# Performance work log

Measured on AMD Instinct MI355X. Metric: run time of the kernel, lower is better.

The kernel has to match this reference:

```python
import jax, jax.numpy as jnp
import numpy as np

BATCH = 16384
NUM_INPUTS = 128
# features = squares (n) + singles (n) + pairs C(n,2)
NUM_FEATS = NUM_INPUTS + NUM_INPUTS + (NUM_INPUTS * (NUM_INPUTS - 1)) // 2  # 8384

# precompute pair index lists (equivalent to itertools.combinations(range(n), 2))
_II, _JJ = np.triu_indices(NUM_INPUTS, k=1)
_II = jnp.asarray(_II)
_JJ = jnp.asarray(_JJ)


def setup_inputs() -> dict:
    key = jax.random.key(0)
    k1, k2 = jax.random.split(key)
    x = jax.random.normal(k1, (BATCH, NUM_INPUTS), dtype=jnp.float32)
    w = jax.random.normal(k2, (NUM_FEATS,), dtype=jnp.float32) * 0.05
    return {"x": x, "w": w}


def reference(x, w):
    # order=2, with_squares=True
    # squares block: o=1 -> inputs**2 / 1**2
    sq = x * x
    # combination order 1: f = 1! -> x / 1
    singles = x
    # combination order 2: f = 2! -> x_i * x_j / 2 for all i<j (combinations order)
    pairs = (x[:, _II] * x[:, _JJ]) * jnp.float32(0.5)
    t = jnp.concatenate([sq, singles, pairs], axis=-1)  # [B, 8384]
    return t * w
```

## Files before the change

### kernel.cpp

```cpp
#include <hip/hip_runtime.h>


constexpr int BATCH   = 16384;
constexpr int NIN     = 128;
constexpr int NFEAT   = NIN + NIN + (NIN * (NIN - 1)) / 2;
constexpr int TPB     = 256;
constexpr int ROWS    = 8;
constexpr int RSTRIDE = 132;
constexpr int KITERS  = (NFEAT + TPB - 1) / TPB;

__device__ __forceinline__ int pair_off(int i) {
    return i * (NIN - 1) - (i * (i - 1)) / 2;
}

__device__ __forceinline__ void decode_f(int f, float w, int& i, int& j, float& ws) {
    if (f < NIN)          { i = f;       j = f;   ws = w; }
    else if (f < 2 * NIN) { i = f - NIN; j = NIN; ws = w; }
    else {
        const int p = f - 2 * NIN;
        float s = sqrtf((float)(65025 - 8 * p));
        int  ii = (int)((255.0f - s) * 0.5f);
        ii = min(max(ii, 0), NIN - 2);
        while (pair_off(ii + 1) <= p) ++ii;
        while (pair_off(ii)     >  p) --ii;
        i = ii; j = ii + 1 + (p - pair_off(ii));
        ws = w * 0.5f;
    }
}

__global__ void setup_kernel(const float* __restrict__ w,
                             float* __restrict__ wsb,
                             unsigned short* __restrict__ tbl) {
    const int f = blockIdx.x * TPB + threadIdx.x;
    if (f >= NFEAT) return;
    int i, j; float ws;
    decode_f(f, w[f], i, j, ws);
    wsb[f] = ws;
    tbl[f] = (unsigned short)((i << 8) | j);
}

template <bool USE_TBL>
__global__ __launch_bounds__(TPB) void cpl_kernel(const float* __restrict__ x,
                                                  const float* __restrict__ w,
                                                  const float* __restrict__ wsb,
                                                  const unsigned short* __restrict__ tbl,
                                                  float* __restrict__ out) {
    __shared__ float xs[ROWS * RSTRIDE];
    const int tid = threadIdx.x;
    const int r0  = blockIdx.x * ROWS;

    {
        const int r = tid >> 5, c = (tid & 31) * 4;
        float4 v = *reinterpret_cast<const float4*>(x + (size_t)(r0 + r) * NIN + c);
        *reinterpret_cast<float4*>(&xs[r * RSTRIDE + c]) = v;
    }
    if (tid < ROWS) xs[tid * RSTRIDE + NIN] = 1.0f;
    __syncthreads();

    unsigned short e_nx = 0; float w_nx = 0.0f;
    if (USE_TBL) { e_nx = tbl[tid]; w_nx = wsb[tid]; }

    for (int k = 0; k < KITERS; ++k) {
        const int f = k * TPB + tid;
        int i, j; float ws;
        if (USE_TBL) {
            const unsigned short e = e_nx; ws = w_nx;
            const int fn = min(f + TPB, NFEAT - 1);
            e_nx = tbl[fn]; w_nx = wsb[fn];
            i = e >> 8; j = e & 255;
        } else {
            if (f < NFEAT) decode_f(f, w[f], i, j, ws);
            else           { i = 0; j = 0; ws = 0.0f; }
        }
        if (f < NFEAT) {
            float* op = out + (size_t)r0 * NFEAT + f;
#pragma unroll
            for (int r = 0; r < ROWS; ++r) {
                const float* xr = &xs[r * RSTRIDE];
                op[(size_t)r * NFEAT] = xr[i] * xr[j] * ws;
            }
        }
    }
}

extern "C" void kernel_launch(void* const* d_in, const int* in_sizes, int n_in,
                              void* d_out, int out_size, void* d_ws, size_t ws_size,
                              hipStream_t stream) {
    const float* x = (const float*)d_in[0];
    const float* w = (const float*)d_in[1];
    float*     out = (float*)d_out;

    const size_t need = (size_t)NFEAT * sizeof(float) + (size_t)NFEAT * sizeof(unsigned short);
    float*          wsb = (float*)d_ws;
    unsigned short* tbl = (unsigned short*)((char*)d_ws + (size_t)NFEAT * sizeof(float));

    const dim3 grid(BATCH / ROWS);

    if (ws_size >= need) {
        setup_kernel<<<(NFEAT + TPB - 1) / TPB, TPB, 0, stream>>>(w, wsb, tbl);
        cpl_kernel<true><<<grid, TPB, 0, stream>>>(x, w, wsb, tbl, out);
    } else {
        cpl_kernel<false><<<grid, TPB, 0, stream>>>(x, w, wsb, tbl, out);
    }
}
```

Measured before the change: 115.5 us.

## Stage index/weight tables in shared memory and process 16 rows per block

Each block now copies the whole feature index table and scaled weights (about 67KB) into LDS, then iterates row-major over 16 batch rows instead of 8. Table lookups therefore come from LDS rather than from global/L2 on every feature iteration, and writes go out row by row. The cost is a large LDS footprint that limits occupancy to a block or two per CU, plus a per-block table copy, which may hurt latency hiding on a store-bound kernel.

```diff
diff --git a/kernel.cpp b/kernel.cpp
--- a/kernel.cpp
+++ b/kernel.cpp
@@ -1,21 +1,19 @@
 #include <hip/hip_runtime.h>
 
 
-constexpr int BATCH   = 16384;
-constexpr int NIN     = 128;
-constexpr int NFEAT   = NIN + NIN + (NIN * (NIN - 1)) / 2;
-constexpr int TPB     = 256;
-constexpr int ROWS    = 8;
-constexpr int RSTRIDE = 132;
-constexpr int KITERS  = (NFEAT + TPB - 1) / TPB;
+constexpr int BATCH = 16384;
+constexpr int NIN   = 128;
+constexpr int NPAIR = NIN * (NIN - 1) / 2;
+constexpr int NFEAT = 2 * NIN + NPAIR;
+constexpr int TPB   = 256;
+constexpr int ROWS  = 16;
+constexpr int RS    = 132;
 
-__device__ __forceinline__ int pair_off(int i) {
-    return i * (NIN - 1) - (i * (i - 1)) / 2;
-}
+__device__ __forceinline__ int pair_off(int i) { return i * (NIN - 1) - (i * (i - 1)) / 2; }
 
 __device__ __forceinline__ void decode_f(int f, float w, int& i, int& j, float& ws) {
     if (f < NIN)          { i = f;       j = f;   ws = w; }
-    else if (f < 2 * NIN) { i = f - NIN; j = NIN; ws = w; }
+    else if (f < 2 * NIN) { i = f - NIN; j = 128; ws = w; }
     else {
         const int p = f - 2 * NIN;
         float s = sqrtf((float)(65025 - 8 * p));
@@ -29,55 +27,71 @@
 }
 
 __global__ void setup_kernel(const float* __restrict__ w,
-                             float* __restrict__ wsb,
-                             unsigned short* __restrict__ tbl) {
+                             unsigned int* __restrict__ gij,
+                             float* __restrict__ gws) {
     const int f = blockIdx.x * TPB + threadIdx.x;
     if (f >= NFEAT) return;
     int i, j; float ws;
     decode_f(f, w[f], i, j, ws);
-    wsb[f] = ws;
-    tbl[f] = (unsigned short)((i << 8) | j);
+    gij[f] = (unsigned int)((i << 8) | j);
+    gws[f] = ws;
 }
 
-template <bool USE_TBL>
+template <bool USE_WS>
 __global__ __launch_bounds__(TPB) void cpl_kernel(const float* __restrict__ x,
                                                   const float* __restrict__ w,
-                                                  const float* __restrict__ wsb,
-                                                  const unsigned short* __restrict__ tbl,
+                                                  const unsigned int* __restrict__ gij,
+                                                  const float* __restrict__ gws,
                                                   float* __restrict__ out) {
-    __shared__ float xs[ROWS * RSTRIDE];
+    __shared__ unsigned int ijs[NFEAT];
+    __shared__ float        wss[NFEAT];
+    __shared__ float        xs[ROWS * RS];
+
     const int tid = threadIdx.x;
     const int r0  = blockIdx.x * ROWS;
 
-    {
-        const int r = tid >> 5, c = (tid & 31) * 4;
-        float4 v = *reinterpret_cast<const float4*>(x + (size_t)(r0 + r) * NIN + c);
-        *reinterpret_cast<float4*>(&xs[r * RSTRIDE + c]) = v;
+#pragma unroll
+    for (int p = 0; p < 2; ++p) {
+        const int idx = p * TPB + tid;
+        const int r = idx >> 5, c4 = (idx & 31) * 4;
+        float4 v = *reinterpret_cast<const float4*>(x + (size_t)(r0 + r) * NIN + c4);
+        *reinterpret_cast<float4*>(&xs[r * RS + c4]) = v;
     }
-    if (tid < ROWS) xs[tid * RSTRIDE + NIN] = 1.0f;
+    if (tid < ROWS) xs[tid * RS + 128] = 1.0f;
+
+    if (USE_WS) {
+        const uint4*  sij = reinterpret_cast<const uint4*>(gij);
+        const float4* sws = reinterpret_cast<const float4*>(gws);
+        uint4*  dij = reinterpret_cast<uint4*>(ijs);
+        float4* dws = reinterpret_cast<float4*>(wss);
+        for (int t = tid; t < NFEAT / 4; t += TPB) {
+            dij[t] = sij[t];
+            dws[t] = sws[t];
+        }
+    } else {
+        for (int f = tid; f < NFEAT; f += TPB) {
+            int i, j; float ws;
+            decode_f(f, w[f], i, j, ws);
+            ijs[f] = (unsigned int)((i << 8) | j);
+            wss[f] = ws;
+        }
+    }
     __syncthreads();
 
-    unsigned short e_nx = 0; float w_nx = 0.0f;
-    if (USE_TBL) { e_nx = tbl[tid]; w_nx = wsb[tid]; }
-
-    for (int k = 0; k < KITERS; ++k) {
-        const int f = k * TPB + tid;
-        int i, j; float ws;
-        if (USE_TBL) {
-            const unsigned short e = e_nx; ws = w_nx;
-            const int fn = min(f + TPB, NFEAT - 1);
-            e_nx = tbl[fn]; w_nx = wsb[fn];
-            i = e >> 8; j = e & 255;
-        } else {
-            if (f < NFEAT) decode_f(f, w[f], i, j, ws);
-            else           { i = 0; j = 0; ws = 0.0f; }
+    for (int r = 0; r < ROWS; ++r) {
+        const float* xr   = &xs[r * RS];
+        float*       orow = out + (size_t)(r0 + r) * NFEAT;
+#pragma unroll 4
+        for (int k = 0; k < 32; ++k) {
+            const int f = k * TPB + tid;
+            const unsigned int e = ijs[f];
+            orow[f] = xr[e >> 8] * xr[e & 255] * wss[f];
         }
-        if (f < NFEAT) {
-            float* op = out + (size_t)r0 * NFEAT + f;
-#pragma unroll
-            for (int r = 0; r < ROWS; ++r) {
-                const float* xr = &xs[r * RSTRIDE];
-                op[(size_t)r * NFEAT] = xr[i] * xr[j] * ws;
+        {
+            const int f = 32 * TPB + tid;
+            if (f < NFEAT) {
+                const unsigned int e = ijs[f];
+                orow[f] = xr[e >> 8] * xr[e & 255] * wss[f];
             }
         }
     }
@@ -90,16 +104,16 @@
     const float* w = (const float*)d_in[1];
     float*     out = (float*)d_out;
 
-    const size_t need = (size_t)NFEAT * sizeof(float) + (size_t)NFEAT * sizeof(unsigned short);
-    float*          wsb = (float*)d_ws;
-    unsigned short* tbl = (unsigned short*)((char*)d_ws + (size_t)NFEAT * sizeof(float));
+    unsigned int* gij = (unsigned int*)d_ws;
+    float*        gws = (float*)((char*)d_ws + (size_t)NFEAT * sizeof(unsigned int));
+    const size_t  need = (size_t)NFEAT * 8;
 
     const dim3 grid(BATCH / ROWS);
 
     if (ws_size >= need) {
-        setup_kernel<<<(NFEAT + TPB - 1) / TPB, TPB, 0, stream>>>(w, wsb, tbl);
-        cpl_kernel<true><<<grid, TPB, 0, stream>>>(x, w, wsb, tbl, out);
+        setup_kernel<<<(NFEAT + TPB - 1) / TPB, TPB, 0, stream>>>(w, gij, gws);
+        cpl_kernel<true><<<grid, TPB, 0, stream>>>(x, w, gij, gws, out);
     } else {
-        cpl_kernel<false><<<grid, TPB, 0, stream>>>(x, w, wsb, tbl, out);
+        cpl_kernel<false><<<grid, TPB, 0, stream>>>(x, w, gij, gws, out);
     }
 }
```

New measurement: 120.7 us. +4.5%, slower.
